# Kernel optimization log

Hardware: AMD Instinct MI355X
Metric: run time of the kernel (lower is better)

Reference implementation:

```python
import jax, jax.numpy as jnp
import numpy as np

B, C, Hsp, Wsp = 16, 256, 64, 64
NUM_HEADS = 8
NORM_GROUPS = 4
EPS = 1e-5


def setup_inputs() -> dict:
    key = jax.random.key(0)
    ks = jax.random.split(key, 6)
    x = jax.random.normal(ks[0], (B, C, Hsp, Wsp), dtype=jnp.float32)
    gn_weight = jnp.ones((C,), dtype=jnp.float32)
    gn_bias = jnp.zeros((C,), dtype=jnp.float32)
    # Conv2d 1x1 kernels == dense matrices over channels
    qkv_weight = jax.random.normal(ks[1], (3 * C, C), dtype=jnp.float32) * (1.0 / np.sqrt(C))
    proj_weight = jax.random.normal(ks[2], (C, C), dtype=jnp.float32) * (1.0 / np.sqrt(C))
    proj_bias = jax.random.normal(ks[3], (C,), dtype=jnp.float32) * 0.01
    return {
        "x": x,
        "gn_weight": gn_weight,
        "gn_bias": gn_bias,
        "qkv_weight": qkv_weight,
        "proj_weight": proj_weight,
        "proj_bias": proj_bias,
    }


def reference(x, gn_weight, gn_bias, qkv_weight, proj_weight, proj_bias):
    b, c, h, w = x.shape
    hd = c // NUM_HEADS  # head dim
    n = h * w            # number of spatial tokens

    # GroupNorm over (c//G, h, w) per group, then per-channel affine
    xg = x.reshape(b, NORM_GROUPS, -1)
    mu = jnp.mean(xg, axis=-1, keepdims=True)
    var = jnp.mean(jnp.square(xg - mu), axis=-1, keepdims=True)
    xn = ((xg - mu) * jax.lax.rsqrt(var + EPS)).reshape(b, c, h, w)
    xn = xn * gn_weight[None, :, None, None] + gn_bias[None, :, None, None]

    # 1x1 conv (no bias) == channel matmul; output channel order matches torch view(b,3,H,d,h,w)
    qkv = jnp.einsum('bchw,oc->bohw', xn, qkv_weight)  # [b, 3c, h, w]
    qkv = qkv.reshape(b, 3, NUM_HEADS, hd, n)
    q, k, v = qkv[:, 0], qkv[:, 1], qkv[:, 2]          # each [b, H, d, n]

    # Linear (kernelized) attention: softmax over keys' token axis
    k = jax.nn.softmax(k, axis=-1)
    att = jnp.einsum('bhdn,bhen->bhde', k, v)          # [b, H, d, d]
    out = jnp.einsum('bhde,bhdn->bhen', att, q)        # [b, H, d, n]
    out = out.reshape(b, c, h, w)

    # Output 1x1 conv with bias
    return jnp.einsum('bchw,oc->bohw', out, proj_weight) + proj_bias[None, :, None, None]
```

## Files before the change

kernel.cpp:

```cpp
#include <hip/hip_runtime.h>
#include <hip/hip_bf16.h>


typedef __attribute__((ext_vector_type(4))) float f32x4;
typedef __attribute__((ext_vector_type(8))) short bf16x8;
typedef __attribute__((ext_vector_type(4))) short s16x4;
typedef __attribute__((ext_vector_type(8))) unsigned short u16x8;

__device__ inline float b2f(unsigned short u) {
  unsigned int x = ((unsigned int)u) << 16;
  float f; __builtin_memcpy(&f, &x, 4); return f;
}
__device__ inline unsigned short f2b(float f) {
  unsigned int x; __builtin_memcpy(&x, &f, 4);
  x += 0x7FFFu + ((x >> 16) & 1u);
  return (unsigned short)(x >> 16);
}

__global__ void __launch_bounds__(256) k_gn_partial(const float* __restrict__ x,
                                                    float* __restrict__ partials) {
  int blk = blockIdx.x;
  int grp = blk >> 4;
  int part = blk & 15;
  const float* base = x + (size_t)grp * 262144 + (size_t)part * 16384;
  int t = threadIdx.x;
  float s = 0.f, s2 = 0.f;
  for (int i = 0; i < 16; ++i) {
    f32x4 v = *(const f32x4*)(base + (size_t)(i * 256 + t) * 4);
    s  += v[0] + v[1] + v[2] + v[3];
    s2 += v[0]*v[0] + v[1]*v[1] + v[2]*v[2] + v[3]*v[3];
  }
  for (int o = 32; o > 0; o >>= 1) { s += __shfl_down(s, o); s2 += __shfl_down(s2, o); }
  __shared__ float ls[4], ls2[4];
  int w = t >> 6;
  if ((t & 63) == 0) { ls[w] = s; ls2[w] = s2; }
  __syncthreads();
  if (t == 0) {
    partials[blk * 2] = ls[0] + ls[1] + ls[2] + ls[3];
    partials[blk * 2 + 1] = ls2[0] + ls2[1] + ls2[2] + ls2[3];
  }
}

__global__ void __launch_bounds__(256) k_finalize(const float* __restrict__ partials,
                                                  float* __restrict__ stats,
                                                  const float* __restrict__ qkvw,
                                                  unsigned short* __restrict__ Wb,
                                                  unsigned short* __restrict__ WqT) {
  int bx = blockIdx.x, t = threadIdx.x;
  if (bx == 0) {
    if (t < 64) {
      float S = 0.f, S2 = 0.f;
      for (int i = 0; i < 16; ++i) { S += partials[(t * 16 + i) * 2]; S2 += partials[(t * 16 + i) * 2 + 1]; }
      float mu = S * (1.f / 262144.f);
      float var = S2 * (1.f / 262144.f) - mu * mu;
      stats[t * 2] = mu;
      stats[t * 2 + 1] = rsqrtf(var + 1e-5f);
    }
  } else if (bx <= 192) {
    int idx = (bx - 1) * 256 + t;
    f32x4 v = *(const f32x4*)(qkvw + (size_t)idx * 4);
    s16x4 o;
    for (int i = 0; i < 4; ++i) o[i] = (short)f2b(v[i]);
    *(s16x4*)(Wb + (size_t)idx * 4) = o;
  } else {
    int bb = bx - 193;
    int c = bb * 16 + (t & 15);
    int d0 = (t >> 4) * 16;
    for (int i = 0; i < 16; ++i) {
      int d = d0 + i;
      WqT[(size_t)c * 256 + d] = f2b(qkvw[(size_t)d * 256 + c]);
    }
  }
}

__global__ void __launch_bounds__(256) k_norm_t(const float* __restrict__ x,
                                                const float* __restrict__ stats,
                                                const float* __restrict__ gamma,
                                                const float* __restrict__ beta,
                                                unsigned short* __restrict__ xnT) {
  int blk = blockIdx.x;
  int b = blk >> 8;
  int tile = blk & 255;
  int ct = tile >> 6;
  int nt = tile & 63;
  int c0 = ct * 64, n0 = nt * 64;
  __shared__ float T[64][65];
  int t = threadIdx.x;
  float mu = stats[(b * 4 + ct) * 2];
  float rs = stats[(b * 4 + ct) * 2 + 1];
  int cl = t >> 2, q4 = t & 3;
  float sc = gamma[c0 + cl] * rs;
  float off = beta[c0 + cl] - mu * sc;
  const float* xr = x + ((size_t)b * 256 + c0 + cl) * 4096 + n0;
  for (int p = 0; p < 4; ++p) {
    int col = p * 16 + q4 * 4;
    f32x4 v = *(const f32x4*)(xr + col);
    for (int i = 0; i < 4; ++i) T[cl][col + i] = v[i] * sc + off;
  }
  __syncthreads();
  int nl = t >> 2, cc = t & 3;
  u16x8 o0, o1;
  for (int i = 0; i < 8; ++i) o0[i] = f2b(T[cc * 16 + i][nl]);
  for (int i = 0; i < 8; ++i) o1[i] = f2b(T[cc * 16 + 8 + i][nl]);
  unsigned short* dst = xnT + ((size_t)b * 4096 + n0 + nl) * 256 + c0 + cc * 16;
  *(u16x8*)dst = o0;
  *(u16x8*)(dst + 8) = o1;
}

__global__ void __launch_bounds__(256, 2) k_attfused(const unsigned short* __restrict__ Wb,
                                                     const unsigned short* __restrict__ xnT,
                                                     float* __restrict__ attg,
                                                     float* __restrict__ rsums) {
  const int bx = blockIdx.x;
  const int b = bx >> 2, ns = bx & 3, h = blockIdx.y;
  const int hb = b * 8 + h;
  const int t = threadIdx.x;
  const int wave = t >> 6, lane = t & 63;
  const int g = lane >> 4, r = lane & 15;
  const int rh = wave >> 1;
  const int ch = wave & 1;
  __shared__ unsigned short XL[64][256];
  __shared__ unsigned short PL[2][32][72];
  __shared__ unsigned short VL[2][32][72];

  const unsigned short* Wrow = Wb + (size_t)(256 + rh * 256 + h * 32) * 256;
  bf16x8 af[2][8];
#pragma unroll
  for (int rt = 0; rt < 2; ++rt)
#pragma unroll
    for (int kt = 0; kt < 8; ++kt)
      af[rt][kt] = *(const bf16x8*)(Wrow + (size_t)(rt * 16 + r) * 256 + kt * 32 + 8 * g);

  const unsigned short* slice = xnT + ((size_t)b * 4096 + ns * 1024) * 256;
  const int swz = t >> 5;
  const unsigned short* gstage = slice + (size_t)swz * 256 + ((t & 31) ^ swz) * 8;
  char* lstage = (char*)&XL[0][0] + ((t >> 6) << 10);
#pragma unroll
  for (int i = 0; i < 8; ++i)
    __builtin_amdgcn_global_load_lds((const void*)(gstage + (size_t)(i * 8) * 256),
                                     (void*)(lstage + i * 4096), 16, 0, 0);

  f32x4 attacc = {0.f, 0.f, 0.f, 0.f};
  float rs[2][4] = {{0.f,0.f,0.f,0.f},{0.f,0.f,0.f,0.f}};
  const char* xl0 = (const char*)&XL[0][0];
  __syncthreads();

  for (int c = 0; c < 16; ++c) {
    const int cur = c & 1;
    bf16x8 bfr[8][2];
#pragma unroll
    for (int kt = 0; kt < 8; ++kt)
#pragma unroll
      for (int ct = 0; ct < 2; ++ct) {
        const int row = ch * 32 + ct * 16 + r;
        const int slot = (kt * 4 + g) ^ (r & 7);
        bfr[kt][ct] = *(const bf16x8*)(xl0 + row * 512 + slot * 16);
      }
    __syncthreads();
    if (c < 15) {
      const unsigned short* gs = gstage + (size_t)(c + 1) * 64 * 256;
#pragma unroll
      for (int i = 0; i < 8; ++i)
        __builtin_amdgcn_global_load_lds((const void*)(gs + (size_t)(i * 8) * 256),
                                         (void*)(lstage + i * 4096), 16, 0, 0);
    }
    f32x4 sacc[2][2] = {};
    __builtin_amdgcn_s_setprio(1);
#pragma unroll
    for (int kt = 0; kt < 8; ++kt) {
      sacc[0][0] = __builtin_amdgcn_mfma_f32_16x16x32_bf16(af[0][kt], bfr[kt][0], sacc[0][0], 0, 0, 0);
      sacc[0][1] = __builtin_amdgcn_mfma_f32_16x16x32_bf16(af[0][kt], bfr[kt][1], sacc[0][1], 0, 0, 0);
      sacc[1][0] = __builtin_amdgcn_mfma_f32_16x16x32_bf16(af[1][kt], bfr[kt][0], sacc[1][0], 0, 0, 0);
      sacc[1][1] = __builtin_amdgcn_mfma_f32_16x16x32_bf16(af[1][kt], bfr[kt][1], sacc[1][1], 0, 0, 0);
    }
    __builtin_amdgcn_s_setprio(0);
    if (rh == 0) {
#pragma unroll
      for (int rt = 0; rt < 2; ++rt)
#pragma unroll
        for (int ct = 0; ct < 2; ++ct)
#pragma unroll
          for (int reg = 0; reg < 4; ++reg) {
            float e = __expf(sacc[rt][ct][reg]);
            rs[rt][reg] += e;
            PL[cur][rt * 16 + 4 * g + reg][ch * 32 + ct * 16 + r] = f2b(e);
          }
    } else {
#pragma unroll
      for (int rt = 0; rt < 2; ++rt)
#pragma unroll
        for (int ct = 0; ct < 2; ++ct)
#pragma unroll
          for (int reg = 0; reg < 4; ++reg)
            VL[cur][rt * 16 + 4 * g + reg][ch * 32 + ct * 16 + r] = f2b(sacc[rt][ct][reg]);
    }
    __syncthreads();
#pragma unroll
    for (int ks = 0; ks < 2; ++ks) {
      bf16x8 pa = *(const bf16x8*)&PL[cur][rh * 16 + r][ks * 32 + 8 * g];
      bf16x8 vb = *(const bf16x8*)&VL[cur][ch * 16 + r][ks * 32 + 8 * g];
      attacc = __builtin_amdgcn_mfma_f32_16x16x32_bf16(pa, vb, attacc, 0, 0, 0);
    }
  }
  float* ab = attg + (size_t)hb * 1024;
#pragma unroll
  for (int reg = 0; reg < 4; ++reg)
    atomicAdd(&ab[(rh * 16 + 4 * g + reg) * 32 + ch * 16 + r], attacc[reg]);
  if (rh == 0) {
#pragma unroll
    for (int rt = 0; rt < 2; ++rt)
#pragma unroll
      for (int reg = 0; reg < 4; ++reg) {
        float v = rs[rt][reg];
        v += __shfl_xor(v, 1); v += __shfl_xor(v, 2);
        v += __shfl_xor(v, 4); v += __shfl_xor(v, 8);
        if (r == 0) atomicAdd(&rsums[hb * 32 + rt * 16 + 4 * g + reg], v);
      }
  }
}

template<bool OUT_BF16, bool ADD_BIAS>
__global__ void __launch_bounds__(256)
k_gemm_bt(const unsigned short* __restrict__ A,
          const unsigned short* __restrict__ B,
          void* __restrict__ Cv,
          const float* __restrict__ bias,
          long sA, long sB, long sC, int ldc) {
  __shared__ unsigned short LA[128][32];
  __shared__ unsigned short LB[128][32];
  const int t = threadIdx.x;
  const unsigned short* Ab = A + (size_t)blockIdx.z * sA + (size_t)blockIdx.x * 128 * 256;
  const unsigned short* Bb = B + (size_t)blockIdx.z * sB + (size_t)blockIdx.y * 128 * 256;
  const int wave = t >> 6, lane = t & 63;
  const int wm = wave >> 1, wn = wave & 1;
  const int g = lane >> 4, r = lane & 15;
  const int rA = t >> 2, sslot = t & 3;
  const int ws0 = 8 * (sslot ^ (rA & 3));
  const int rslot = 8 * (g ^ (r & 3));
  const unsigned short* ag = Ab + (size_t)rA * 256 + 8 * sslot;
  const unsigned short* bg = Bb + (size_t)rA * 256 + 8 * sslot;
  u16x8 pa0 = *(const u16x8*)(ag);
  u16x8 pa1 = *(const u16x8*)(ag + 64 * 256);
  u16x8 pb0 = *(const u16x8*)(bg);
  u16x8 pb1 = *(const u16x8*)(bg + 64 * 256);
  f32x4 acc[4][4] = {};
  for (int kt = 0; kt < 8; ++kt) {
    if (kt) __syncthreads();
    *(u16x8*)&LA[rA][ws0] = pa0;  *(u16x8*)&LA[rA + 64][ws0] = pa1;
    *(u16x8*)&LB[rA][ws0] = pb0;  *(u16x8*)&LB[rA + 64][ws0] = pb1;
    __syncthreads();
    if (kt < 7) {
      int off = (kt + 1) * 32;
      pa0 = *(const u16x8*)(ag + off);  pa1 = *(const u16x8*)(ag + 64 * 256 + off);
      pb0 = *(const u16x8*)(bg + off);  pb1 = *(const u16x8*)(bg + 64 * 256 + off);
    }
    bf16x8 af[4], bfr[4];
    for (int i = 0; i < 4; ++i) {
      af[i]  = *(const bf16x8*)&LA[wm * 64 + i * 16 + r][rslot];
      bfr[i] = *(const bf16x8*)&LB[wn * 64 + i * 16 + r][rslot];
    }
    for (int mi = 0; mi < 4; ++mi)
      for (int ni = 0; ni < 4; ++ni)
        acc[mi][ni] = __builtin_amdgcn_mfma_f32_16x16x32_bf16(af[mi], bfr[ni], acc[mi][ni], 0, 0, 0);
  }
  const int m0 = blockIdx.x * 128 + wm * 64;
  const int n0 = blockIdx.y * 128 + wn * 64;
  if (OUT_BF16) {
    unsigned short* C = (unsigned short*)Cv + (size_t)blockIdx.z * sC;
    for (int mi = 0; mi < 4; ++mi)
      for (int ni = 0; ni < 4; ++ni) {
        int row = m0 + mi * 16 + 4 * g;
        int col = n0 + ni * 16 + r;
        for (int reg = 0; reg < 4; ++reg)
          C[(size_t)(row + reg) * ldc + col] = f2b(acc[mi][ni][reg]);
      }
  } else {
    float* C = (float*)Cv + (size_t)blockIdx.z * sC;
    for (int mi = 0; mi < 4; ++mi)
      for (int ni = 0; ni < 4; ++ni) {
        int row = m0 + mi * 16 + 4 * g;
        int col = n0 + ni * 16 + r;
        for (int reg = 0; reg < 4; ++reg) {
          float v = acc[mi][ni][reg];
          if (ADD_BIAS) v += bias[row + reg];
          C[(size_t)(row + reg) * ldc + col] = v;
        }
      }
  }
}

__global__ void __launch_bounds__(256) k_makeM(const float* __restrict__ attg,
                                               const float* __restrict__ rsums,
                                               const float* __restrict__ projw,
                                               unsigned short* __restrict__ Mb) {
  int blk = blockIdx.x;
  int b = blk >> 3, h = blk & 7;
  __shared__ float attL[32][33];
  __shared__ float invs[32];
  int t = threadIdx.x;
  if (t < 32) invs[t] = 1.f / rsums[blk * 32 + t];
  const float* asrc = attg + (size_t)blk * 1024;
  {
    f32x4 v = *(const f32x4*)(asrc + (size_t)t * 4);
    int idx = t * 4;
    for (int i = 0; i < 4; ++i) attL[(idx + i) >> 5][(idx + i) & 31] = v[i];
  }
  __syncthreads();
  float pw[32];
  const float* ps = projw + (size_t)t * 256 + h * 32;
  for (int i = 0; i < 8; ++i) {
    f32x4 v = *(const f32x4*)(ps + i * 4);
    pw[i * 4 + 0] = v[0]; pw[i * 4 + 1] = v[1]; pw[i * 4 + 2] = v[2]; pw[i * 4 + 3] = v[3];
  }
  unsigned short* dst = Mb + ((size_t)b * 256 + t) * 256 + h * 32;
  for (int dd = 0; dd < 32; ++dd) {
    float s = 0.f;
    for (int e = 0; e < 32; ++e) s += pw[e] * attL[dd][e];
    dst[dd] = f2b(s * invs[dd]);
  }
}

__global__ void __launch_bounds__(256) k_gemm_final(const unsigned short* __restrict__ M2,
                                                    const unsigned short* __restrict__ xnT,
                                                    float* __restrict__ out,
                                                    const float* __restrict__ bias) {
  const int nt = blockIdx.x, b = blockIdx.y;
  const unsigned short* Ab = M2 + (size_t)b * 65536;
  const unsigned short* Bb = xnT + ((size_t)b * 4096 + nt * 64) * 256;
  float* Cb = out + (size_t)b * 1048576 + (size_t)nt * 64;
  __shared__ unsigned short LB[2][64][32];
  const int t = threadIdx.x;
  const int wave = t >> 6, lane = t & 63, g = lane >> 4, r = lane & 15;
  const int srow = t >> 2, sslot = t & 3;
  const int ws0 = 8 * (sslot ^ (srow & 3));
  const int rslot = 8 * (g ^ (r & 3));
  const unsigned short* bg = Bb + (size_t)srow * 256 + 8 * sslot;
  const unsigned short* ar = Ab + (size_t)(wave * 64 + r) * 256 + 8 * g;
  u16x8 pb = *(const u16x8*)bg;
  f32x4 acc[4][4] = {};
  for (int kt = 0; kt < 8; ++kt) {
    const int cur = kt & 1;
    *(u16x8*)&LB[cur][srow][ws0] = pb;
    __syncthreads();
    if (kt < 7) pb = *(const u16x8*)(bg + (kt + 1) * 32);
    bf16x8 af[4], bfr[4];
#pragma unroll
    for (int mi = 0; mi < 4; ++mi)
      af[mi] = *(const bf16x8*)(ar + (size_t)(mi * 16) * 256 + kt * 32);
#pragma unroll
    for (int ni = 0; ni < 4; ++ni)
      bfr[ni] = *(const bf16x8*)&LB[cur][ni * 16 + r][rslot];
#pragma unroll
    for (int mi = 0; mi < 4; ++mi)
#pragma unroll
      for (int ni = 0; ni < 4; ++ni)
        acc[mi][ni] = __builtin_amdgcn_mfma_f32_16x16x32_bf16(af[mi], bfr[ni], acc[mi][ni], 0, 0, 0);
  }
#pragma unroll
  for (int mi = 0; mi < 4; ++mi) {
    const int row = wave * 64 + mi * 16 + 4 * g;
#pragma unroll
    for (int ni = 0; ni < 4; ++ni)
#pragma unroll
      for (int reg = 0; reg < 4; ++reg)
        Cb[(size_t)(row + reg) * 4096 + ni * 16 + r] = acc[mi][ni][reg] + bias[row + reg];
  }
}

extern "C" void kernel_launch(void* const* d_in, const int* in_sizes, int n_in,
                              void* d_out, int out_size, void* d_ws, size_t ws_size,
                              hipStream_t stream) {
  (void)in_sizes; (void)n_in; (void)out_size; (void)ws_size;
  const float* x     = (const float*)d_in[0];
  const float* gn_w  = (const float*)d_in[1];
  const float* gn_b  = (const float*)d_in[2];
  const float* qkvw  = (const float*)d_in[3];
  const float* projw = (const float*)d_in[4];
  const float* projb = (const float*)d_in[5];

  char* ws = (char*)d_ws;
  float*          partials = (float*)(ws);
  float*          stats    = (float*)(ws + 8192);
  unsigned short* Wb       = (unsigned short*)(ws + 16384);
  unsigned short* Mb       = (unsigned short*)(ws + 409600);
  float*          attg     = (float*)(ws + 2506752);
  float*          rsums    = (float*)(ws + 3031040);
  unsigned short* WqT      = (unsigned short*)(ws + 3047424);
  unsigned short* M2       = (unsigned short*)(ws + 3178496);
  unsigned short* xnT      = (unsigned short*)(ws + 8388608);

  k_gn_partial<<<1024, 256, 0, stream>>>(x, partials);
  k_finalize<<<209, 256, 0, stream>>>(partials, stats, qkvw, Wb, WqT);
  k_norm_t<<<4096, 256, 0, stream>>>(x, stats, gn_w, gn_b, xnT);
  (void)hipMemsetAsync(attg, 0, 540672, stream);
  k_attfused<<<dim3(64, 8), 256, 0, stream>>>(Wb, xnT, attg, rsums);
  k_makeM<<<128, 256, 0, stream>>>(attg, rsums, projw, Mb);
  k_gemm_bt<true, false><<<dim3(2, 2, 16), 256, 0, stream>>>(
      Mb, WqT, (void*)M2, nullptr, 65536L, 0L, 65536L, 256);
  k_gemm_final<<<dim3(64, 16), 256, 0, stream>>>(M2, xnT, (float*)d_out, projb);
}
```

Before: 205.7 us.

## Double-buffer X tile in attention kernel and fold log2e into K weights

The fused attention kernel now keeps two LDS buffers for the X tile. The next chunk's global-to-LDS load is issued before the current chunk is read, which removes the barrier that separated the fragment reads from the refill. The P/V exchange buffers are now single-buffered and written from registers after an extra barrier. Separately, K weights are pre-scaled by log2(e) during bf16 conversion so the kernel can use exp2f instead of __expf. The trade-off is about twice the X-tile LDS footprint, which may pressure the two-blocks-per-CU occupancy target, plus one added barrier per iteration.

Result: slower. 210.2 us (+2.2%).

```diff
diff --git a/kernel.cpp b/kernel.cpp
--- a/kernel.cpp
+++ b/kernel.cpp
@@ -58,9 +58,11 @@
     }
   } else if (bx <= 192) {
     int idx = (bx - 1) * 256 + t;
+    int row = idx >> 6;
+    float scl = (row >= 256 && row < 512) ? 1.4426950408889634f : 1.0f;
     f32x4 v = *(const f32x4*)(qkvw + (size_t)idx * 4);
     s16x4 o;
-    for (int i = 0; i < 4; ++i) o[i] = (short)f2b(v[i]);
+    for (int i = 0; i < 4; ++i) o[i] = (short)f2b(v[i] * scl);
     *(s16x4*)(Wb + (size_t)idx * 4) = o;
   } else {
     int bb = bx - 193;
@@ -119,9 +121,9 @@
   const int g = lane >> 4, r = lane & 15;
   const int rh = wave >> 1;
   const int ch = wave & 1;
-  __shared__ unsigned short XL[64][256];
-  __shared__ unsigned short PL[2][32][72];
-  __shared__ unsigned short VL[2][32][72];
+  __shared__ unsigned short XL[2][64][256];
+  __shared__ unsigned short PL[32][72];
+  __shared__ unsigned short VL[32][72];
 
   const unsigned short* Wrow = Wb + (size_t)(256 + rh * 256 + h * 32) * 256;
   bf16x8 af[2][8];
@@ -134,19 +136,27 @@
   const unsigned short* slice = xnT + ((size_t)b * 4096 + ns * 1024) * 256;
   const int swz = t >> 5;
   const unsigned short* gstage = slice + (size_t)swz * 256 + ((t & 31) ^ swz) * 8;
-  char* lstage = (char*)&XL[0][0] + ((t >> 6) << 10);
+  char* lbase = (char*)&XL[0][0][0] + ((t >> 6) << 10);
 #pragma unroll
   for (int i = 0; i < 8; ++i)
     __builtin_amdgcn_global_load_lds((const void*)(gstage + (size_t)(i * 8) * 256),
-                                     (void*)(lstage + i * 4096), 16, 0, 0);
+                                     (void*)(lbase + i * 4096), 16, 0, 0);
 
   f32x4 attacc = {0.f, 0.f, 0.f, 0.f};
-  float rs[2][4] = {{0.f,0.f,0.f,0.f},{0.f,0.f,0.f,0.f}};
-  const char* xl0 = (const char*)&XL[0][0];
+  float rsm[2][4] = {{0.f,0.f,0.f,0.f},{0.f,0.f,0.f,0.f}};
   __syncthreads();
 
   for (int c = 0; c < 16; ++c) {
-    const int cur = c & 1;
+    const int cur = c & 1, nxt = cur ^ 1;
+    if (c < 15) {
+      const unsigned short* gs = gstage + (size_t)(c + 1) * 64 * 256;
+      char* ld = lbase + (size_t)nxt * 32768;
+#pragma unroll
+      for (int i = 0; i < 8; ++i)
+        __builtin_amdgcn_global_load_lds((const void*)(gs + (size_t)(i * 8) * 256),
+                                         (void*)(ld + i * 4096), 16, 0, 0);
+    }
+    const char* xl0 = (const char*)&XL[cur][0][0];
     bf16x8 bfr[8][2];
 #pragma unroll
     for (int kt = 0; kt < 8; ++kt)
@@ -156,14 +166,6 @@
         const int slot = (kt * 4 + g) ^ (r & 7);
         bfr[kt][ct] = *(const bf16x8*)(xl0 + row * 512 + slot * 16);
       }
-    __syncthreads();
-    if (c < 15) {
-      const unsigned short* gs = gstage + (size_t)(c + 1) * 64 * 256;
-#pragma unroll
-      for (int i = 0; i < 8; ++i)
-        __builtin_amdgcn_global_load_lds((const void*)(gs + (size_t)(i * 8) * 256),
-                                         (void*)(lstage + i * 4096), 16, 0, 0);
-    }
     f32x4 sacc[2][2] = {};
     __builtin_amdgcn_s_setprio(1);
 #pragma unroll
@@ -174,6 +176,7 @@
       sacc[1][1] = __builtin_amdgcn_mfma_f32_16x16x32_bf16(af[1][kt], bfr[kt][1], sacc[1][1], 0, 0, 0);
     }
     __builtin_amdgcn_s_setprio(0);
+    unsigned short ov[2][2][4];
     if (rh == 0) {
 #pragma unroll
       for (int rt = 0; rt < 2; ++rt)
@@ -181,9 +184,9 @@
         for (int ct = 0; ct < 2; ++ct)
 #pragma unroll
           for (int reg = 0; reg < 4; ++reg) {
-            float e = __expf(sacc[rt][ct][reg]);
-            rs[rt][reg] += e;
-            PL[cur][rt * 16 + 4 * g + reg][ch * 32 + ct * 16 + r] = f2b(e);
+            float e = exp2f(sacc[rt][ct][reg]);
+            rsm[rt][reg] += e;
+            ov[rt][ct][reg] = f2b(e);
           }
     } else {
 #pragma unroll
@@ -192,13 +195,24 @@
         for (int ct = 0; ct < 2; ++ct)
 #pragma unroll
           for (int reg = 0; reg < 4; ++reg)
-            VL[cur][rt * 16 + 4 * g + reg][ch * 32 + ct * 16 + r] = f2b(sacc[rt][ct][reg]);
+            ov[rt][ct][reg] = f2b(sacc[rt][ct][reg]);
     }
     __syncthreads();
+    {
+      unsigned short (*dstL)[72] = (rh == 0) ? PL : VL;
+#pragma unroll
+      for (int rt = 0; rt < 2; ++rt)
+#pragma unroll
+        for (int ct = 0; ct < 2; ++ct)
+#pragma unroll
+          for (int reg = 0; reg < 4; ++reg)
+            dstL[rt * 16 + 4 * g + reg][ch * 32 + ct * 16 + r] = ov[rt][ct][reg];
+    }
+    __syncthreads();
 #pragma unroll
     for (int ks = 0; ks < 2; ++ks) {
-      bf16x8 pa = *(const bf16x8*)&PL[cur][rh * 16 + r][ks * 32 + 8 * g];
-      bf16x8 vb = *(const bf16x8*)&VL[cur][ch * 16 + r][ks * 32 + 8 * g];
+      bf16x8 pa = *(const bf16x8*)&PL[rh * 16 + r][ks * 32 + 8 * g];
+      bf16x8 vb = *(const bf16x8*)&VL[ch * 16 + r][ks * 32 + 8 * g];
       attacc = __builtin_amdgcn_mfma_f32_16x16x32_bf16(pa, vb, attacc, 0, 0, 0);
     }
   }
@@ -211,7 +225,7 @@
     for (int rt = 0; rt < 2; ++rt)
 #pragma unroll
       for (int reg = 0; reg < 4; ++reg) {
-        float v = rs[rt][reg];
+        float v = rsm[rt][reg];
         v += __shfl_xor(v, 1); v += __shfl_xor(v, 2);
         v += __shfl_xor(v, 4); v += __shfl_xor(v, 8);
         if (r == 0) atomicAdd(&rsums[hb * 32 + rt * 16 + 4 * g + reg], v);
```
